# Kernel optimization log

Measured on AMD Instinct MI355X. Metric: run time of the kernel, lower is better.

The kernel has to match this reference:

```python
import jax, jax.numpy as jnp
import numpy as np

N, E, G = 30000, 480000, 64
IN, MID, HEADS, OUT = 256, (64, 64, 128), 8, 13


def _tconv(x, src, dst, ea, qw, qb, kw, kb, vw, vb, ew, sw, sb, heads, n):
    # PyG TransformerConv (concat=True, root_weight=True, beta=False), eval mode
    d = qw.shape[1] // heads
    q = (x @ qw + qb)[dst].reshape(-1, heads, d)   # [E,H,d] query at target
    k = (x @ kw + kb)[src].reshape(-1, heads, d)   # [E,H,d] key at source
    v = (x @ vw + vb)[src].reshape(-1, heads, d)   # [E,H,d] value at source
    e = (ea @ ew).reshape(-1, heads, d)            # [E,H,d] edge embedding (no bias)
    k = k + e
    a = (q * k).sum(-1) / jnp.sqrt(jnp.asarray(d, x.dtype))   # [E,H]
    amax = jax.ops.segment_max(a, dst, num_segments=n)        # segment softmax over in-edges
    ex = jnp.exp(a - amax[dst])
    den = jax.ops.segment_sum(ex, dst, num_segments=n)
    alpha = ex / den[dst]
    out = jax.ops.segment_sum((v + e) * alpha[..., None], dst, num_segments=n)
    out = out.reshape(n, heads * d)
    return out + x @ sw + sb                        # root/skip connection


def _mk(key, shape):
    return jax.random.normal(key, shape, dtype=jnp.float32) * 0.05


def setup_inputs() -> dict:
    key = jax.random.key(0)
    ks = iter(jax.random.split(key, 40))
    inp = {
        "x": jax.random.normal(next(ks), (N, IN), dtype=jnp.float32),
        "edge_index": jax.random.randint(next(ks), (2, E), 0, N, dtype=jnp.int64),
        "edge_attr": jax.random.normal(next(ks), (E, 1), dtype=jnp.float32),
        "batch": jnp.sort(jax.random.randint(next(ks), (N,), 0, G, dtype=jnp.int64)),
    }
    # conv1: in=256 -> heads=8, d=64 (out 512)
    o1 = HEADS * MID[0]
    inp.update(q1w=_mk(next(ks), (IN, o1)), q1b=_mk(next(ks), (o1,)),
               k1w=_mk(next(ks), (IN, o1)), k1b=_mk(next(ks), (o1,)),
               v1w=_mk(next(ks), (IN, o1)), v1b=_mk(next(ks), (o1,)),
               e1w=_mk(next(ks), (1, o1)),
               s1w=_mk(next(ks), (IN, o1)), s1b=_mk(next(ks), (o1,)))
    # conv2: in=512 -> heads=4, d=64 (out 256)
    h2, i2 = HEADS // 2, o1
    o2 = h2 * MID[1]
    inp.update(q2w=_mk(next(ks), (i2, o2)), q2b=_mk(next(ks), (o2,)),
               k2w=_mk(next(ks), (i2, o2)), k2b=_mk(next(ks), (o2,)),
               v2w=_mk(next(ks), (i2, o2)), v2b=_mk(next(ks), (o2,)),
               e2w=_mk(next(ks), (1, o2)),
               s2w=_mk(next(ks), (i2, o2)), s2b=_mk(next(ks), (o2,)))
    # conv3: in=256 -> heads=1, d=128
    i3, o3 = o2, MID[2]
    inp.update(q3w=_mk(next(ks), (i3, o3)), q3b=_mk(next(ks), (o3,)),
               k3w=_mk(next(ks), (i3, o3)), k3b=_mk(next(ks), (o3,)),
               v3w=_mk(next(ks), (i3, o3)), v3b=_mk(next(ks), (o3,)),
               e3w=_mk(next(ks), (1, o3)),
               s3w=_mk(next(ks), (i3, o3)), s3b=_mk(next(ks), (o3,)))
    inp.update(lw=_mk(next(ks), (MID[2], OUT)), lb=_mk(next(ks), (OUT,)))
    return inp


def reference(x, edge_index, edge_attr, batch,
              q1w, q1b, k1w, k1b, v1w, v1b, e1w, s1w, s1b,
              q2w, q2b, k2w, k2b, v2w, v2b, e2w, s2w, s2b,
              q3w, q3b, k3w, k3b, v3w, v3b, e3w, s3w, s3b,
              lw, lb):
    src, dst = edge_index[0], edge_index[1]
    h = _tconv(x, src, dst, edge_attr, q1w, q1b, k1w, k1b, v1w, v1b, e1w, s1w, s1b, HEADS, N)
    h = jax.nn.relu(h)
    h = _tconv(h, src, dst, edge_attr, q2w, q2b, k2w, k2b, v2w, v2b, e2w, s2w, s2b, HEADS // 2, N)
    h = jax.nn.relu(h)
    h = _tconv(h, src, dst, edge_attr, q3w, q3b, k3w, k3b, v3w, v3b, e3w, s3w, s3b, 1, N)
    # global mean pool over graphs
    s = jax.ops.segment_sum(h, batch, num_segments=G)
    cnt = jax.ops.segment_sum(jnp.ones((N,), h.dtype), batch, num_segments=G)
    pooled = s / jnp.maximum(cnt, 1.0)[:, None]
    return pooled @ lw + lb
```

## Files before the change

kernel.cpp:

```cpp
#include <hip/hip_runtime.h>
#include <hip/hip_bf16.h>
#include <cstdint>

#define NN 30000
#define EE 480000
#define GG 64

typedef __attribute__((ext_vector_type(8))) short bf16x8;
typedef __attribute__((ext_vector_type(4))) float float4v;
typedef __attribute__((ext_vector_type(4))) unsigned short ushort4v;

static __device__ inline unsigned short f2bf(float f) {
    unsigned u = __float_as_uint(f);
    unsigned r = (u + 0x7fff + ((u >> 16) & 1)) >> 16;
    return (unsigned short)r;
}
static __device__ inline float bf2f(unsigned short u) {
    return __uint_as_float(((unsigned)u) << 16);
}

__global__ void count_deg_k(const int* __restrict__ ei, int* __restrict__ deg) {
    int e = blockIdx.x * 256 + threadIdx.x;
    if (e < EE) atomicAdd(&deg[ei[EE + e]], 1);
}

__global__ __launch_bounds__(1024) void scan_excl_k(const int* __restrict__ deg,
                                                    int* __restrict__ basep) {
    constexpr int CH = (NN + 1024) / 1024 + 1;
    __shared__ int buf[1024];
    int t = threadIdx.x;
    int b0 = t * CH;
    int loc[CH];
    int s = 0;
#pragma unroll
    for (int i = 0; i < CH; i++) {
        int idx = b0 + i;
        int v = (idx < NN) ? deg[idx] : 0;
        loc[i] = s;
        s += v;
    }
    buf[t] = s;
    __syncthreads();
    for (int off = 1; off < 1024; off <<= 1) {
        int tv = (t >= off) ? buf[t - off] : 0;
        __syncthreads();
        buf[t] += tv;
        __syncthreads();
    }
    int base = (t > 0) ? buf[t - 1] : 0;
#pragma unroll
    for (int i = 0; i < CH; i++) {
        int idx = b0 + i;
        if (idx <= NN) basep[idx] = base + loc[i];
    }
}

__global__ void fill_csr_k(const int* __restrict__ ei, const float* __restrict__ ea,
                           const int* __restrict__ basep, int* __restrict__ cnt,
                           int* __restrict__ csrc, float* __restrict__ cea) {
    int e = blockIdx.x * 256 + threadIdx.x;
    if (e < EE) {
        int d = ei[EE + e];
        int pos = basep[d] + atomicAdd(&cnt[d], 1);
        csrc[pos] = ei[e];
        cea[pos] = ea[e];
    }
}

__global__ void gbound_k(const int* __restrict__ batch, int* __restrict__ gstart) {
    int i = blockIdx.x * 256 + threadIdx.x;
    if (i >= NN) return;
    int cur = batch[i];
    if (i == 0) {
        for (int g = 0; g <= cur; ++g) gstart[g] = 0;
    } else {
        int prev = batch[i - 1];
        for (int g = prev + 1; g <= cur; ++g) gstart[g] = i;
    }
    if (i == NN - 1) {
        for (int g = cur + 1; g <= GG; ++g) gstart[g] = NN;
    }
}

struct PrepDesc { const float* src; void* dst; int rows; int cols; int blk0; int mode; };
#define NDESC 25
struct PrepArgs { PrepDesc d[NDESC]; };

__global__ __launch_bounds__(256) void prep_k(PrepArgs args) {
    int b = blockIdx.x;
    PrepDesc dd = args.d[0];
#pragma unroll
    for (int i = 1; i < NDESC; i++)
        if (b >= args.d[i].blk0) dd = args.d[i];
    int rel = b - dd.blk0;
    int total = dd.rows * dd.cols;
    int base = rel * 1024 + threadIdx.x;
    if (dd.mode == 0) {
        unsigned short* dst = (unsigned short*)dd.dst;
        for (int j = 0; j < 4; j++) {
            int i = base + j * 256;
            if (i < total) dst[i] = f2bf(dd.src[i]);
        }
    } else if (dd.mode == 1) {
        unsigned short* dst = (unsigned short*)dd.dst;
        for (int j = 0; j < 4; j++) {
            int i = base + j * 256;
            if (i < total) {
                int n = i / dd.rows, k = i - n * dd.rows;
                dst[i] = f2bf(dd.src[(size_t)k * dd.cols + n]);
            }
        }
    } else {
        float* dst = (float*)dd.dst;
        for (int j = 0; j < 4; j++) {
            int i = base + j * 256;
            if (i < total) dst[i] = dd.src[i];
        }
    }
}

__global__ __launch_bounds__(256) void gemm_bf16_k(
    const unsigned short* __restrict__ A, const unsigned short* __restrict__ Wt,
    const float* __restrict__ bias, unsigned short* __restrict__ C,
    int M, int K, int N) {
    __shared__ unsigned short As[2][4096];
    __shared__ unsigned short Bs[2][4096];
    int tid = threadIdx.x;
    int lane = tid & 63, wid = tid >> 6;
    int wm = wid >> 1, wn = wid & 1;
    int row0 = blockIdx.y * 128, n0 = blockIdx.x * 128;

    float4v acc[4][4];
#pragma unroll
    for (int i = 0; i < 4; i++)
#pragma unroll
        for (int j = 0; j < 4; j++) acc[i][j] = (float4v)0.f;

    auto stage = [&](int buf, int k0) {
#pragma unroll
        for (int i = 0; i < 2; ++i) {
            int chunkbase = i * 256 + wid * 64;
            int chunk = chunkbase + lane;
            int r = chunk & 127, kc = chunk >> 7;
            int rowA = row0 + r; if (rowA >= M) rowA = M - 1;
            const unsigned short* ga = A + (size_t)rowA * K + (k0 + kc * 8);
            __builtin_amdgcn_global_load_lds(
                (const __attribute__((address_space(1))) void*)ga,
                (__attribute__((address_space(3))) void*)(As[buf] + (size_t)chunkbase * 8),
                16, 0, 0);
            const unsigned short* gb = Wt + (size_t)(n0 + r) * K + (k0 + kc * 8);
            __builtin_amdgcn_global_load_lds(
                (const __attribute__((address_space(1))) void*)gb,
                (__attribute__((address_space(3))) void*)(Bs[buf] + (size_t)chunkbase * 8),
                16, 0, 0);
        }
    };

    stage(0, 0);
    asm volatile("s_waitcnt vmcnt(0)" ::: "memory");
    __syncthreads();

    int NT = K >> 5;
    for (int t = 0; t < NT; ++t) {
        int b = t & 1;
        if (t + 1 < NT) stage(b ^ 1, (t + 1) << 5);
        bf16x8 af[4], bfr[4];
#pragma unroll
        for (int mi = 0; mi < 4; mi++)
            af[mi] = *(const bf16x8*)(As[b] + ((lane >> 4) * 128 + wm * 64 + mi * 16 + (lane & 15)) * 8);
#pragma unroll
        for (int ni = 0; ni < 4; ni++)
            bfr[ni] = *(const bf16x8*)(Bs[b] + ((lane >> 4) * 128 + wn * 64 + ni * 16 + (lane & 15)) * 8);
#pragma unroll
        for (int mi = 0; mi < 4; mi++)
#pragma unroll
            for (int ni = 0; ni < 4; ni++)
                acc[mi][ni] = __builtin_amdgcn_mfma_f32_16x16x32_bf16(
                    bfr[ni], af[mi], acc[mi][ni], 0, 0, 0);
        asm volatile("s_waitcnt vmcnt(0)" ::: "memory");
        __syncthreads();
    }

    float4v bias4[4];
#pragma unroll
    for (int ni = 0; ni < 4; ni++)
        bias4[ni] = *(const float4v*)&bias[n0 + wn * 64 + ni * 16 + (lane >> 4) * 4];
#pragma unroll
    for (int mi = 0; mi < 4; mi++) {
        int row = row0 + wm * 64 + mi * 16 + (lane & 15);
        if (row < M) {
#pragma unroll
            for (int ni = 0; ni < 4; ni++) {
                int colb = n0 + wn * 64 + ni * 16 + (lane >> 4) * 4;
                ushort4v pk;
#pragma unroll
                for (int r = 0; r < 4; r++) pk[r] = f2bf(acc[mi][ni][r] + bias4[ni][r]);
                *(ushort4v*)(C + (size_t)row * N + colb) = pk;
            }
        }
    }
}

template <int VEC>
__device__ inline void loadbf(const unsigned short* __restrict__ p, float (&r)[VEC]) {
    if constexpr (VEC == 2) {
        unsigned v = *(const unsigned*)p;
        r[0] = __uint_as_float(v << 16);
        r[1] = __uint_as_float(v & 0xffff0000u);
    } else if constexpr (VEC == 4) {
        uint2 v = *(const uint2*)p;
        r[0] = __uint_as_float(v.x << 16); r[1] = __uint_as_float(v.x & 0xffff0000u);
        r[2] = __uint_as_float(v.y << 16); r[3] = __uint_as_float(v.y & 0xffff0000u);
    } else {
        uint4 v = *(const uint4*)p;
        r[0] = __uint_as_float(v.x << 16); r[1] = __uint_as_float(v.x & 0xffff0000u);
        r[2] = __uint_as_float(v.y << 16); r[3] = __uint_as_float(v.y & 0xffff0000u);
        r[4] = __uint_as_float(v.z << 16); r[5] = __uint_as_float(v.z & 0xffff0000u);
        r[6] = __uint_as_float(v.w << 16); r[7] = __uint_as_float(v.w & 0xffff0000u);
    }
}
template <int VEC>
__device__ inline void loadf32(const float* __restrict__ p, float (&r)[VEC]) {
    if constexpr (VEC == 2) {
        float2 t = *reinterpret_cast<const float2*>(p);
        r[0] = t.x; r[1] = t.y;
    } else {
#pragma unroll
        for (int i = 0; i < VEC; i += 4) {
            float4 t = *reinterpret_cast<const float4*>(p + i);
            r[i] = t.x; r[i + 1] = t.y; r[i + 2] = t.z; r[i + 3] = t.w;
        }
    }
}
template <int VEC>
__device__ inline void storebf(unsigned short* __restrict__ p, const float (&r)[VEC]) {
    unsigned w[VEC / 2];
#pragma unroll
    for (int i = 0; i < VEC / 2; i++)
        w[i] = (unsigned)f2bf(r[2 * i]) | ((unsigned)f2bf(r[2 * i + 1]) << 16);
    if constexpr (VEC == 2) *(unsigned*)p = w[0];
    else if constexpr (VEC == 4) *(uint2*)p = make_uint2(w[0], w[1]);
    else *(uint4*)p = make_uint4(w[0], w[1], w[2], w[3]);
}

template <int H, int D, bool RELU>
__global__ __launch_bounds__(256) void aggregate_k(
    const unsigned short* __restrict__ QKVS, int SR,
    const float* __restrict__ ew,
    const int* __restrict__ rowptr, const int* __restrict__ csrc,
    const float* __restrict__ cea, unsigned short* __restrict__ Hout) {
    constexpr int F = H * D;
    constexpr int VEC = F / 64;
    constexpr int L = 64 / H;
    int lane = threadIdx.x & 63;
    int node = blockIdx.x * 4 + (threadIdx.x >> 6);
    if (node >= NN) return;

    const unsigned short* qrow = QKVS + (size_t)node * SR;
    float q[VEC], ewv[VEC], acc[VEC];
    loadbf<VEC>(qrow + lane * VEC, q);
    loadf32<VEC>(ew + lane * VEC, ewv);
#pragma unroll
    for (int i = 0; i < VEC; i++) acc[i] = 0.f;

    float den = 0.f;
    const float isd = rsqrtf((float)D);
    int beg = rowptr[node], end = rowptr[node + 1];

    float kA[VEC], vA[VEC], eA = 0.f;
    float kB[VEC], vB[VEC], eB = 0.f;
    if (beg < end) {
        int s = csrc[beg]; eA = cea[beg];
        const unsigned short* b = QKVS + (size_t)s * SR + F;
        loadbf<VEC>(b + lane * VEC, kA);
        loadbf<VEC>(b + F + lane * VEC, vA);
    }
    if (beg + 1 < end) {
        int s = csrc[beg + 1]; eB = cea[beg + 1];
        const unsigned short* b = QKVS + (size_t)s * SR + F;
        loadbf<VEC>(b + lane * VEC, kB);
        loadbf<VEC>(b + F + lane * VEC, vB);
    }

    for (int j = beg; j < end; j += 2) {
        {
            float t[VEC], p = 0.f;
#pragma unroll
            for (int i = 0; i < VEC; i++) { t[i] = eA * ewv[i]; p += q[i] * (kA[i] + t[i]); }
#pragma unroll
            for (int off = 1; off < L; off <<= 1) p += __shfl_xor(p, off, 64);
            float w = __expf(fminf(p * isd, 30.f));
            den += w;
#pragma unroll
            for (int i = 0; i < VEC; i++) acc[i] += w * (vA[i] + t[i]);
        }
        if (j + 2 < end) {
            int s = csrc[j + 2]; eA = cea[j + 2];
            const unsigned short* b = QKVS + (size_t)s * SR + F;
            loadbf<VEC>(b + lane * VEC, kA);
            loadbf<VEC>(b + F + lane * VEC, vA);
        }
        if (j + 1 < end) {
            float t[VEC], p = 0.f;
#pragma unroll
            for (int i = 0; i < VEC; i++) { t[i] = eB * ewv[i]; p += q[i] * (kB[i] + t[i]); }
#pragma unroll
            for (int off = 1; off < L; off <<= 1) p += __shfl_xor(p, off, 64);
            float w = __expf(fminf(p * isd, 30.f));
            den += w;
#pragma unroll
            for (int i = 0; i < VEC; i++) acc[i] += w * (vB[i] + t[i]);
        }
        if (j + 3 < end) {
            int s = csrc[j + 3]; eB = cea[j + 3];
            const unsigned short* b = QKVS + (size_t)s * SR + F;
            loadbf<VEC>(b + lane * VEC, kB);
            loadbf<VEC>(b + F + lane * VEC, vB);
        }
    }

    float rden = (den > 0.f) ? 1.f / den : 0.f;
    float sv[VEC];
    loadbf<VEC>(qrow + 3 * F + lane * VEC, sv);
    float o[VEC];
#pragma unroll
    for (int i = 0; i < VEC; i++) {
        float v = acc[i] * rden + sv[i];
        o[i] = RELU ? fmaxf(v, 0.f) : v;
    }
    storebf<VEC>(Hout + (size_t)node * F + lane * VEC, o);
}

__global__ __launch_bounds__(256) void pool_head_k(
    const unsigned short* __restrict__ h3, const int* __restrict__ gstart,
    const float* __restrict__ lw, const float* __restrict__ lb,
    float* __restrict__ out) {
    __shared__ float part[256];
    __shared__ float pooled[128];
    int g = blockIdx.x;
    int beg = gstart[g], end = gstart[g + 1];
    int d = threadIdx.x & 127, half = threadIdx.x >> 7;
    float s = 0.f;
    for (int node = beg + half; node < end; node += 2)
        s += bf2f(h3[(size_t)node * 128 + d]);
    part[threadIdx.x] = s;
    __syncthreads();
    if (threadIdx.x < 128) {
        float cnt = fmaxf((float)(end - beg), 1.0f);
        pooled[threadIdx.x] = (part[threadIdx.x] + part[threadIdx.x + 128]) / cnt;
    }
    __syncthreads();
    if (threadIdx.x < 13) {
        float acc = lb[threadIdx.x];
        for (int dd = 0; dd < 128; ++dd)
            acc += pooled[dd] * lw[dd * 13 + threadIdx.x];
        out[g * 13 + threadIdx.x] = acc;
    }
}

__global__ void ws_fail_k(float* __restrict__ out, int n) {
    int i = blockIdx.x * 256 + threadIdx.x;
    if (i < n) out[i] = -12345.0f;
}

extern "C" void kernel_launch(void* const* d_in, const int* in_sizes, int n_in,
                              void* d_out, int out_size, void* d_ws, size_t ws_size,
                              hipStream_t stream) {
    const float* x   = (const float*)d_in[0];
    const int*   ei  = (const int*)d_in[1];
    const float* ea  = (const float*)d_in[2];
    const int*   bat = (const int*)d_in[3];
    const float* W1[4] = {(const float*)d_in[4], (const float*)d_in[6], (const float*)d_in[8], (const float*)d_in[11]};
    const float* B1[4] = {(const float*)d_in[5], (const float*)d_in[7], (const float*)d_in[9], (const float*)d_in[12]};
    const float* e1w = (const float*)d_in[10];
    const float* W2[4] = {(const float*)d_in[13], (const float*)d_in[15], (const float*)d_in[17], (const float*)d_in[20]};
    const float* B2[4] = {(const float*)d_in[14], (const float*)d_in[16], (const float*)d_in[18], (const float*)d_in[21]};
    const float* e2w = (const float*)d_in[19];
    const float* W3[4] = {(const float*)d_in[22], (const float*)d_in[24], (const float*)d_in[26], (const float*)d_in[29]};
    const float* B3[4] = {(const float*)d_in[23], (const float*)d_in[25], (const float*)d_in[27], (const float*)d_in[30]};
    const float* e3w = (const float*)d_in[28];
    const float* lw  = (const float*)d_in[31];
    const float* lb  = (const float*)d_in[32];

    char* wsb = (char*)d_ws;
    size_t off = 0;
    auto alloc_b = [&](size_t bytes) {
        void* p = wsb + off;
        off += (bytes + 255) & ~(size_t)255;
        return p;
    };
    unsigned short* xb   = (unsigned short*)alloc_b((size_t)NN * 256 * 2);
    unsigned short* Wc1  = (unsigned short*)alloc_b((size_t)2048 * 256 * 2);
    float*          bc1  = (float*)alloc_b(2048 * 4);
    unsigned short* Wc2  = (unsigned short*)alloc_b((size_t)1024 * 512 * 2);
    float*          bc2  = (float*)alloc_b(1024 * 4);
    unsigned short* Wc3  = (unsigned short*)alloc_b((size_t)512 * 256 * 2);
    float*          bc3  = (float*)alloc_b(512 * 4);
    unsigned short* QKVS = (unsigned short*)alloc_b((size_t)NN * 2048 * 2);
    unsigned short* H1   = (unsigned short*)alloc_b((size_t)NN * 512 * 2);
    unsigned short* H2   = (unsigned short*)alloc_b((size_t)NN * 256 * 2);
    unsigned short* H3   = (unsigned short*)alloc_b((size_t)NN * 128 * 2);
    int*   basep  = (int*)alloc_b((NN + 1) * 4);
    int*   csrc   = (int*)alloc_b((size_t)EE * 4);
    float* cea    = (float*)alloc_b((size_t)EE * 4);
    int*   gstart = (int*)alloc_b((GG + 1) * 4);
    size_t zstart = off;
    int*   deg    = (int*)alloc_b(NN * 4);
    int*   cnt    = (int*)alloc_b(NN * 4);
    size_t zbytes = off - zstart;

    if (ws_size < off) {
        ws_fail_k<<<(out_size + 255) / 256, 256, 0, stream>>>((float*)d_out, out_size);
        return;
    }

    hipMemsetAsync(wsb + zstart, 0, zbytes, stream);

    PrepArgs pa;
    int blk = 0, di = 0;
    auto add = [&](const float* src, void* dst, int rows, int cols, int mode) {
        pa.d[di].src = src; pa.d[di].dst = dst;
        pa.d[di].rows = rows; pa.d[di].cols = cols;
        pa.d[di].mode = mode; pa.d[di].blk0 = blk;
        blk += (rows * cols + 1023) / 1024;
        di++;
    };
    add(x, xb, NN * 256, 1, 0);
    for (int s = 0; s < 4; s++) add(W1[s], Wc1 + (size_t)s * 512 * 256, 256, 512, 1);
    for (int s = 0; s < 4; s++) add(B1[s], bc1 + s * 512, 512, 1, 2);
    for (int s = 0; s < 4; s++) add(W2[s], Wc2 + (size_t)s * 256 * 512, 512, 256, 1);
    for (int s = 0; s < 4; s++) add(B2[s], bc2 + s * 256, 256, 1, 2);
    for (int s = 0; s < 4; s++) add(W3[s], Wc3 + (size_t)s * 128 * 256, 256, 128, 1);
    for (int s = 0; s < 4; s++) add(B3[s], bc3 + s * 128, 128, 1, 2);
    prep_k<<<blk, 256, 0, stream>>>(pa);

    int eblocks = (EE + 255) / 256;
    count_deg_k<<<eblocks, 256, 0, stream>>>(ei, deg);
    scan_excl_k<<<1, 1024, 0, stream>>>(deg, basep);
    fill_csr_k<<<eblocks, 256, 0, stream>>>(ei, ea, basep, cnt, csrc, cea);
    gbound_k<<<(NN + 255) / 256, 256, 0, stream>>>(bat, gstart);

    int mblocks = (NN + 127) / 128;
    gemm_bf16_k<<<dim3(2048 / 128, mblocks), 256, 0, stream>>>(xb, Wc1, bc1, QKVS, NN, 256, 2048);
    aggregate_k<8, 64, true><<<NN / 4, 256, 0, stream>>>(QKVS, 2048, e1w, basep, csrc, cea, H1);
    gemm_bf16_k<<<dim3(1024 / 128, mblocks), 256, 0, stream>>>(H1, Wc2, bc2, QKVS, NN, 512, 1024);
    aggregate_k<4, 64, true><<<NN / 4, 256, 0, stream>>>(QKVS, 1024, e2w, basep, csrc, cea, H2);
    gemm_bf16_k<<<dim3(512 / 128, mblocks), 256, 0, stream>>>(H2, Wc3, bc3, QKVS, NN, 256, 512);
    aggregate_k<1, 128, false><<<NN / 4, 256, 0, stream>>>(QKVS, 512, e3w, basep, csrc, cea, H3);

    pool_head_k<<<GG, 256, 0, stream>>>(H3, gstart, lw, lb, (float*)d_out);
}
```

Baseline: 823.9 us.

## Deepen edge prefetch to four in aggregation and remap GEMM tiles per XCD

The aggregation kernel now keeps four in-flight neighbor K/V loads instead of two, and holds them as raw packed bf16 registers that are unpacked only when used. This is meant to hide more gather latency per wavefront and to keep register pressure from unpacked floats down. Separately, the GEMM remaps block IDs so that consecutive tiles land on the same XCD, which is meant to improve L2 reuse on the chiplet layout. The cost is more live registers for the deeper prefetch, which could reduce occupancy.

```diff
diff --git a/kernel.cpp b/kernel.cpp
--- a/kernel.cpp
+++ b/kernel.cpp
@@ -128,7 +128,15 @@
     int tid = threadIdx.x;
     int lane = tid & 63, wid = tid >> 6;
     int wm = wid >> 1, wn = wid & 1;
-    int row0 = blockIdx.y * 128, n0 = blockIdx.x * 128;
+
+    int gx = gridDim.x;
+    int T = gx * gridDim.y;
+    int lid = blockIdx.y * gx + blockIdx.x;
+    int qq = T >> 3, rr = T & 7;
+    int xcd = lid & 7, pos = lid >> 3;
+    int tile = ((xcd < rr) ? xcd * (qq + 1) : rr * (qq + 1) + (xcd - rr) * qq) + pos;
+    int by = tile / gx, bx = tile - by * gx;
+    int row0 = by * 128, n0 = bx * 128;
 
     float4v acc[4][4];
 #pragma unroll
@@ -201,23 +209,29 @@
     }
 }
 
+template <int VEC> struct RawVec;
+template <> struct RawVec<2> { using T = unsigned; };
+template <> struct RawVec<4> { using T = uint2; };
+template <> struct RawVec<8> { using T = uint4; };
+
+static __device__ inline void unpackr(unsigned v, float (&r)[2]) {
+    r[0] = __uint_as_float(v << 16); r[1] = __uint_as_float(v & 0xffff0000u);
+}
+static __device__ inline void unpackr(uint2 v, float (&r)[4]) {
+    r[0] = __uint_as_float(v.x << 16); r[1] = __uint_as_float(v.x & 0xffff0000u);
+    r[2] = __uint_as_float(v.y << 16); r[3] = __uint_as_float(v.y & 0xffff0000u);
+}
+static __device__ inline void unpackr(uint4 v, float (&r)[8]) {
+    r[0] = __uint_as_float(v.x << 16); r[1] = __uint_as_float(v.x & 0xffff0000u);
+    r[2] = __uint_as_float(v.y << 16); r[3] = __uint_as_float(v.y & 0xffff0000u);
+    r[4] = __uint_as_float(v.z << 16); r[5] = __uint_as_float(v.z & 0xffff0000u);
+    r[6] = __uint_as_float(v.w << 16); r[7] = __uint_as_float(v.w & 0xffff0000u);
+}
+
 template <int VEC>
 __device__ inline void loadbf(const unsigned short* __restrict__ p, float (&r)[VEC]) {
-    if constexpr (VEC == 2) {
-        unsigned v = *(const unsigned*)p;
-        r[0] = __uint_as_float(v << 16);
-        r[1] = __uint_as_float(v & 0xffff0000u);
-    } else if constexpr (VEC == 4) {
-        uint2 v = *(const uint2*)p;
-        r[0] = __uint_as_float(v.x << 16); r[1] = __uint_as_float(v.x & 0xffff0000u);
-        r[2] = __uint_as_float(v.y << 16); r[3] = __uint_as_float(v.y & 0xffff0000u);
-    } else {
-        uint4 v = *(const uint4*)p;
-        r[0] = __uint_as_float(v.x << 16); r[1] = __uint_as_float(v.x & 0xffff0000u);
-        r[2] = __uint_as_float(v.y << 16); r[3] = __uint_as_float(v.y & 0xffff0000u);
-        r[4] = __uint_as_float(v.z << 16); r[5] = __uint_as_float(v.z & 0xffff0000u);
-        r[6] = __uint_as_float(v.w << 16); r[7] = __uint_as_float(v.w & 0xffff0000u);
-    }
+    typename RawVec<VEC>::T v = *(const typename RawVec<VEC>::T*)p;
+    unpackr(v, r);
 }
 template <int VEC>
 __device__ inline void loadf32(const float* __restrict__ p, float (&r)[VEC]) {
@@ -252,6 +266,7 @@
     constexpr int F = H * D;
     constexpr int VEC = F / 64;
     constexpr int L = 64 / H;
+    using RawT = typename RawVec<VEC>::T;
     int lane = threadIdx.x & 63;
     int node = blockIdx.x * 4 + (threadIdx.x >> 6);
     if (node >= NN) return;
@@ -267,55 +282,48 @@
     const float isd = rsqrtf((float)D);
     int beg = rowptr[node], end = rowptr[node + 1];
 
-    float kA[VEC], vA[VEC], eA = 0.f;
-    float kB[VEC], vB[VEC], eB = 0.f;
-    if (beg < end) {
-        int s = csrc[beg]; eA = cea[beg];
-        const unsigned short* b = QKVS + (size_t)s * SR + F;
-        loadbf<VEC>(b + lane * VEC, kA);
-        loadbf<VEC>(b + F + lane * VEC, vA);
-    }
-    if (beg + 1 < end) {
-        int s = csrc[beg + 1]; eB = cea[beg + 1];
-        const unsigned short* b = QKVS + (size_t)s * SR + F;
-        loadbf<VEC>(b + lane * VEC, kB);
-        loadbf<VEC>(b + F + lane * VEC, vB);
-    }
-
-    for (int j = beg; j < end; j += 2) {
-        {
-            float t[VEC], p = 0.f;
-#pragma unroll
-            for (int i = 0; i < VEC; i++) { t[i] = eA * ewv[i]; p += q[i] * (kA[i] + t[i]); }
-#pragma unroll
-            for (int off = 1; off < L; off <<= 1) p += __shfl_xor(p, off, 64);
-            float w = __expf(fminf(p * isd, 30.f));
-            den += w;
-#pragma unroll
-            for (int i = 0; i < VEC; i++) acc[i] += w * (vA[i] + t[i]);
+    RawT k0r, k1r, k2r, k3r, v0r, v1r, v2r, v3r;
+    float e0, e1, e2, e3;
+    auto fetch = [&](int j, RawT& kr, RawT& vr, float& ea) {
+        int s = csrc[j]; ea = cea[j];
+        const unsigned short* b = QKVS + (size_t)s * SR + F + lane * VEC;
+        kr = *(const RawT*)b;
+        vr = *(const RawT*)(b + F);
+    };
+    auto process = [&](RawT kr, RawT vr, float ea) {
+        float kv[VEC], vv[VEC], t[VEC];
+        unpackr(kr, kv);
+        unpackr(vr, vv);
+        float p = 0.f;
+#pragma unroll
+        for (int i = 0; i < VEC; i++) { t[i] = ea * ewv[i]; p += q[i] * (kv[i] + t[i]); }
+#pragma unroll
+        for (int off = 1; off < L; off <<= 1) p += __shfl_xor(p, off, 64);
+        float w = __expf(fminf(p * isd, 30.f));
+        den += w;
+#pragma unroll
+        for (int i = 0; i < VEC; i++) acc[i] += w * (vv[i] + t[i]);
+    };
+
+    if (beg + 0 < end) fetch(beg + 0, k0r, v0r, e0);
+    if (beg + 1 < end) fetch(beg + 1, k1r, v1r, e1);
+    if (beg + 2 < end) fetch(beg + 2, k2r, v2r, e2);
+    if (beg + 3 < end) fetch(beg + 3, k3r, v3r, e3);
+
+    for (int j = beg; j < end; j += 4) {
+        process(k0r, v0r, e0);
+        if (j + 4 < end) fetch(j + 4, k0r, v0r, e0);
+        if (j + 1 < end) {
+            process(k1r, v1r, e1);
+            if (j + 5 < end) fetch(j + 5, k1r, v1r, e1);
         }
         if (j + 2 < end) {
-            int s = csrc[j + 2]; eA = cea[j + 2];
-            const unsigned short* b = QKVS + (size_t)s * SR + F;
-            loadbf<VEC>(b + lane * VEC, kA);
-            loadbf<VEC>(b + F + lane * VEC, vA);
-        }
-        if (j + 1 < end) {
-            float t[VEC], p = 0.f;
-#pragma unroll
-            for (int i = 0; i < VEC; i++) { t[i] = eB * ewv[i]; p += q[i] * (kB[i] + t[i]); }
-#pragma unroll
-            for (int off = 1; off < L; off <<= 1) p += __shfl_xor(p, off, 64);
-            float w = __expf(fminf(p * isd, 30.f));
-            den += w;
-#pragma unroll
-            for (int i = 0; i < VEC; i++) acc[i] += w * (vB[i] + t[i]);
+            process(k2r, v2r, e2);
+            if (j + 6 < end) fetch(j + 6, k2r, v2r, e2);
         }
         if (j + 3 < end) {
-            int s = csrc[j + 3]; eB = cea[j + 3];
-            const unsigned short* b = QKVS + (size_t)s * SR + F;
-            loadbf<VEC>(b + lane * VEC, kB);
-            loadbf<VEC>(b + F + lane * VEC, vB);
+            process(k3r, v3r, e3);
+            if (j + 7 < end) fetch(j + 7, k3r, v3r, e3);
         }
     }
 
```

After: 793.9 us. -3.6%, faster.
